# Performance work log

Hardware: AMD Instinct MI355X
Metric: run time of the kernel (lower is better)

Reference implementation:

```python
import jax, jax.numpy as jnp
import numpy as np

D = 1024  # input_size
H = 1024  # hidden_size
B = 128
R = 512


def _lin(x, W, b):
    return x @ W + b


def setup_inputs() -> dict:
    key = jax.random.key(0)
    ks = jax.random.split(key, 20)
    s = 0.02
    inp = {
        "V": jax.random.normal(ks[0], (B, R, D), jnp.float32),
        "s_t": jax.random.normal(ks[1], (B, D), jnp.float32),
        "h_t": jax.random.normal(ks[2], (B, D), jnp.float32),
        # weights stored [in, out] (y = x @ W + b)
        "Wv": jax.random.normal(ks[3], (D, H), jnp.float32) * s,
        "bv": jnp.zeros((H,), jnp.float32),
        "Wsp": jax.random.normal(ks[4], (D, D), jnp.float32) * s,
        "bsp": jnp.zeros((D,), jnp.float32),
        "Wsa": jax.random.normal(ks[5], (D, H), jnp.float32) * s,
        "bsa": jnp.zeros((H,), jnp.float32),
        "Whp": jax.random.normal(ks[6], (D, D), jnp.float32) * s,
        "bhp": jnp.zeros((D,), jnp.float32),
        "Wha": jax.random.normal(ks[7], (D, H), jnp.float32) * s,
        "bha": jnp.zeros((H,), jnp.float32),
        "Wal": jax.random.normal(ks[8], (H, 1), jnp.float32) * s,
        "bal": jnp.zeros((1,), jnp.float32),
        "Wcp": jax.random.normal(ks[9], (D, D), jnp.float32) * s,
        "bcp": jnp.zeros((D,), jnp.float32),
    }
    return inp


def reference(V, s_t, h_t, Wv, bv, Wsp, bsp, Wsa, bsa, Whp, bhp, Wha, bha, Wal, bal, Wcp, bcp):
    v_embed = jax.nn.relu(_lin(V, Wv, bv))           # [B,R,H]
    s_proj = jax.nn.relu(_lin(s_t, Wsp, bsp))        # [B,D]
    s_att = _lin(s_proj, Wsa, bsa)                   # [B,H]
    h_proj = jnp.tanh(_lin(h_t, Whp, bhp))           # [B,D]
    h_att = _lin(h_proj, Wha, bha)                   # [B,H]
    regions = jnp.concatenate([V, s_proj[:, None, :]], axis=1)           # [B,R+1,D]
    regions_att = jnp.concatenate([v_embed, s_att[:, None, :]], axis=1)  # [B,R+1,H]
    alpha_input = jnp.tanh(regions_att + h_att[:, None, :])              # [B,R+1,H]
    scores = (_lin(alpha_input, Wal, bal)).squeeze(-1)                   # [B,R+1]
    alpha = jax.nn.softmax(scores, axis=1)                               # [B,R+1]
    context = jnp.einsum("br,brd->bd", alpha, regions)                   # [B,D]
    z_t = jnp.tanh(_lin(context + h_proj, Wcp, bcp))                     # [B,D]
    return z_t
```

## Files before the change

### kernel.cpp

```cpp
#include <hip/hip_runtime.h>


typedef __bf16 bf16x8 __attribute__((ext_vector_type(8)));
typedef float floatx4 __attribute__((ext_vector_type(4)));

__device__ __forceinline__ float tanh_fast(float x) {
    x = fminf(10.0f, fmaxf(-10.0f, x));
    float e = exp2f(x * 2.885390081777927f);
    return (e - 1.0f) * __builtin_amdgcn_rcpf(e + 1.0f);
}

__global__ __launch_bounds__(256) void conv_k(
    const float* __restrict__ V, __bf16* __restrict__ Vb) {
    const size_t i = ((size_t)blockIdx.x * 256 + threadIdx.x) * 8;
    const float4 a = *reinterpret_cast<const float4*>(V + i);
    const float4 b = *reinterpret_cast<const float4*>(V + i + 4);
    bf16x8 o;
    o[0] = (__bf16)a.x; o[1] = (__bf16)a.y;
    o[2] = (__bf16)a.z; o[3] = (__bf16)a.w;
    o[4] = (__bf16)b.x; o[5] = (__bf16)b.y;
    o[6] = (__bf16)b.z; o[7] = (__bf16)b.w;
    *reinterpret_cast<bf16x8*>(Vb + i) = o;
}

__global__ __launch_bounds__(256) void wvt_kernel(
    const float* __restrict__ Wv, __bf16* __restrict__ WvT) {
    __shared__ float tile[64][65];
    const int k0 = blockIdx.x * 64, n0 = blockIdx.y * 64;
    const int c = threadIdx.x & 63, r = threadIdx.x >> 6;
#pragma unroll
    for (int i = 0; i < 16; ++i)
        tile[r + i * 4][c] = Wv[(size_t)(k0 + r + i * 4) * 1024 + n0 + c];
    __syncthreads();
#pragma unroll
    for (int i = 0; i < 16; ++i)
        WvT[(size_t)(n0 + r + i * 4) * 1024 + k0 + c] =
            (__bf16)tile[c][r + i * 4];
}

__global__ __launch_bounds__(512) void small_gemm_k(
    const float* __restrict__ A0, const float* __restrict__ W0,
    const float* __restrict__ b0, float* __restrict__ C0, int act0,
    const float* __restrict__ A1, const float* __restrict__ W1,
    const float* __restrict__ b1, float* __restrict__ C1, int act1) {
    const float* A; const float* W; const float* bs; float* C; int act;
    if (blockIdx.z == 0) { A = A0; W = W0; bs = b0; C = C0; act = act0; }
    else                 { A = A1; W = W1; bs = b1; C = C1; act = act1; }
    __shared__ float red[3][8][128];
    const int tid = threadIdx.x;
    const int nl = tid & 127, kq = tid >> 7;
    const int n = blockIdx.x * 128 + nl;
    const int m0 = blockIdx.y * 8;
    const float* Ab = A + m0 * 1024;
    float acc[8] = {};
    const int kbeg = kq * 256, kend = kbeg + 256;
#pragma unroll 4
    for (int k = kbeg; k < kend; ++k) {
        float w = W[(size_t)k * 1024 + n];
#pragma unroll
        for (int mi = 0; mi < 8; ++mi)
            acc[mi] = fmaf(Ab[mi * 1024 + k], w, acc[mi]);
    }
    if (kq > 0) {
#pragma unroll
        for (int mi = 0; mi < 8; ++mi) red[kq - 1][mi][nl] = acc[mi];
    }
    __syncthreads();
    if (kq == 0) {
        float bias = bs[n];
#pragma unroll
        for (int mi = 0; mi < 8; ++mi) {
            float v = acc[mi] + red[0][mi][nl] + red[1][mi][nl] +
                      red[2][mi][nl] + bias;
            if (act == 1) v = fmaxf(v, 0.0f);
            else if (act == 2) v = tanh_fast(v);
            C[(size_t)(m0 + mi) * 1024 + n] = v;
        }
    }
}

__global__ __launch_bounds__(256, 3) void score_gemm_k(
    const __bf16* __restrict__ Vb, const __bf16* __restrict__ WvT,
    const float* __restrict__ bv, const float* __restrict__ h_att,
    const float* __restrict__ Wal, float* __restrict__ scores) {
    __shared__ __bf16 As[2][128 * 32];
    __shared__ __bf16 Bs[2][128 * 32];

    const int tid = threadIdx.x;
    const int bid = blockIdx.x;
    const int xcd = bid & 7;
    const int j = bid >> 3;
    const int mtile = xcd * 64 + (j >> 3);
    const int ntile = j & 7;
    const int m0 = mtile * 128, n0 = ntile * 128;
    const int wid = tid >> 6, lane = tid & 63;
    const int wm = wid & 1, wn = wid >> 1;
    const int lcol = lane & 15, quad = lane >> 4;

    floatx4 acc[4][4] = {};

    const int grow = tid >> 2;
    const int kg = (tid & 3) ^ ((grow >> 1) & 3);
    const __bf16* ap0 = Vb + (size_t)(m0 + grow) * 1024 + kg * 8;
    const __bf16* bp0 = WvT + (size_t)(n0 + grow) * 1024 + kg * 8;

    auto dma = [&](int buf, int k0) {
        __builtin_amdgcn_global_load_lds(
            (const __attribute__((address_space(1))) void*)(ap0 + k0),
            (__attribute__((address_space(3))) void*)(&As[buf][tid * 8]),
            16, 0, 0);
        __builtin_amdgcn_global_load_lds(
            (const __attribute__((address_space(1))) void*)(ap0 + 64 * 1024 + k0),
            (__attribute__((address_space(3))) void*)(&As[buf][(256 + tid) * 8]),
            16, 0, 0);
        __builtin_amdgcn_global_load_lds(
            (const __attribute__((address_space(1))) void*)(bp0 + k0),
            (__attribute__((address_space(3))) void*)(&Bs[buf][tid * 8]),
            16, 0, 0);
        __builtin_amdgcn_global_load_lds(
            (const __attribute__((address_space(1))) void*)(bp0 + 64 * 1024 + k0),
            (__attribute__((address_space(3))) void*)(&Bs[buf][(256 + tid) * 8]),
            16, 0, 0);
    };

    dma(0, 0);

    int aoff[4], boff[4];
#pragma unroll
    for (int i = 0; i < 4; ++i) {
        int r = wm * 64 + i * 16 + lcol;
        aoff[i] = r * 32 + ((quad ^ ((r >> 1) & 3)) * 8);
        int n = wn * 64 + i * 16 + lcol;
        boff[i] = n * 32 + ((quad ^ ((n >> 1) & 3)) * 8);
    }
    __syncthreads();

    for (int kk = 0; kk < 32; ++kk) {
        const int cur = kk & 1, nxt = cur ^ 1;
        if (kk < 31) dma(nxt, (kk + 1) * 32);
        bf16x8 af[4], bfr[4];
#pragma unroll
        for (int i = 0; i < 4; ++i) {
            af[i] = *reinterpret_cast<const bf16x8*>(&As[cur][aoff[i]]);
            bfr[i] = *reinterpret_cast<const bf16x8*>(&Bs[cur][boff[i]]);
        }
#pragma unroll
        for (int mi = 0; mi < 4; ++mi)
#pragma unroll
            for (int ni = 0; ni < 4; ++ni)
                acc[mi][ni] = __builtin_amdgcn_mfma_f32_16x16x32_bf16(
                    af[mi], bfr[ni], acc[mi][ni], 0, 0, 0);
        __syncthreads();
    }

    const int b = m0 >> 9;
    float wal[4], hat[4], bvv[4];
#pragma unroll
    for (int ni = 0; ni < 4; ++ni) {
        int n = n0 + wn * 64 + ni * 16 + lcol;
        wal[ni] = Wal[n];
        hat[ni] = h_att[b * 1024 + n];
        bvv[ni] = bv[n];
    }
    float p[16];
#pragma unroll
    for (int mi = 0; mi < 4; ++mi) {
#pragma unroll
        for (int rg = 0; rg < 4; ++rg) {
            float s = 0.f;
#pragma unroll
            for (int ni = 0; ni < 4; ++ni) {
                float x = acc[mi][ni][rg] + bvv[ni];
                x = fmaxf(x, 0.f);
                s = fmaf(wal[ni], tanh_fast(x + hat[ni]), s);
            }
            p[mi * 4 + rg] = s;
        }
    }
#pragma unroll
    for (int off = 1; off < 16; off <<= 1) {
#pragma unroll
        for (int i = 0; i < 16; ++i) p[i] += __shfl_xor(p[i], off, 64);
    }
    if (lcol == 0) {
#pragma unroll
        for (int mi = 0; mi < 4; ++mi)
#pragma unroll
            for (int rg = 0; rg < 4; ++rg) {
                int row = m0 + wm * 64 + mi * 16 + quad * 4 + rg;
                atomicAdd(&scores[b * 513 + (row & 511)], p[mi * 4 + rg]);
            }
    }
}

__global__ __launch_bounds__(256, 3) void score_gemm_fb(
    const float* __restrict__ V, const __bf16* __restrict__ WvT,
    const float* __restrict__ bv, const float* __restrict__ h_att,
    const float* __restrict__ Wal, float* __restrict__ scores) {
    __shared__ __bf16 As[2][128 * 40];
    __shared__ __bf16 Bs[2][128 * 32];

    const int tid = threadIdx.x;
    const int bid = blockIdx.x;
    const int xcd = bid & 7;
    const int j = bid >> 3;
    const int mtile = xcd * 64 + (j >> 3);
    const int ntile = j & 7;
    const int m0 = mtile * 128, n0 = ntile * 128;
    const int wid = tid >> 6, lane = tid & 63;
    const int wm = wid & 1, wn = wid >> 1;
    const int lcol = lane & 15, quad = lane >> 4;

    floatx4 acc[4][4] = {};

    const int am = tid >> 1;
    const int ak = (tid & 1) * 16;
    const float* aptr = V + (size_t)(m0 + am) * 1024 + ak;

    const int g0n = tid >> 2, g0ks = tid & 3;
    const int g1n = (256 + tid) >> 2, g1ks = tid & 3;
    const int g0kg = g0ks ^ ((g0n >> 1) & 3);
    const int g1kg = g1ks ^ ((g1n >> 1) & 3);
    const __bf16* bp0 = WvT + (size_t)(n0 + g0n) * 1024 + g0kg * 8;
    const __bf16* bp1 = WvT + (size_t)(n0 + g1n) * 1024 + g1kg * 8;

    auto stage_A = [&](int buf, float4 f0, float4 f1, float4 f2, float4 f3) {
        bf16x8 u0, u1;
        u0[0] = (__bf16)f0.x; u0[1] = (__bf16)f0.y;
        u0[2] = (__bf16)f0.z; u0[3] = (__bf16)f0.w;
        u0[4] = (__bf16)f1.x; u0[5] = (__bf16)f1.y;
        u0[6] = (__bf16)f1.z; u0[7] = (__bf16)f1.w;
        u1[0] = (__bf16)f2.x; u1[1] = (__bf16)f2.y;
        u1[2] = (__bf16)f2.z; u1[3] = (__bf16)f2.w;
        u1[4] = (__bf16)f3.x; u1[5] = (__bf16)f3.y;
        u1[6] = (__bf16)f3.z; u1[7] = (__bf16)f3.w;
        __bf16* awr = &As[buf][am * 40 + ak];
        *reinterpret_cast<bf16x8*>(awr) = u0;
        *reinterpret_cast<bf16x8*>(awr + 8) = u1;
    };
    auto dma_B = [&](int buf, int k0) {
        __builtin_amdgcn_global_load_lds(
            (const __attribute__((address_space(1))) void*)(bp0 + k0),
            (__attribute__((address_space(3))) void*)(&Bs[buf][tid * 8]),
            16, 0, 0);
        __builtin_amdgcn_global_load_lds(
            (const __attribute__((address_space(1))) void*)(bp1 + k0),
            (__attribute__((address_space(3))) void*)(&Bs[buf][(256 + tid) * 8]),
            16, 0, 0);
    };

    dma_B(0, 0);
    {
        const float4* fp = reinterpret_cast<const float4*>(aptr);
        stage_A(0, fp[0], fp[1], fp[2], fp[3]);
    }
    __syncthreads();

    for (int kk = 0; kk < 32; ++kk) {
        const int cur = kk & 1, nxt = cur ^ 1;
        float4 f0, f1, f2, f3;
        const bool pf = (kk < 31);
        if (pf) {
            dma_B(nxt, (kk + 1) * 32);
            const float4* fp =
                reinterpret_cast<const float4*>(aptr + (kk + 1) * 32);
            f0 = fp[0]; f1 = fp[1]; f2 = fp[2]; f3 = fp[3];
        }
        bf16x8 af[4], bfr[4];
#pragma unroll
        for (int mi = 0; mi < 4; ++mi)
            af[mi] = *reinterpret_cast<const bf16x8*>(
                &As[cur][(wm * 64 + mi * 16 + lcol) * 40 + quad * 8]);
#pragma unroll
        for (int ni = 0; ni < 4; ++ni) {
            int n = wn * 64 + ni * 16 + lcol;
            int ks = quad ^ ((n >> 1) & 3);
            bfr[ni] = *reinterpret_cast<const bf16x8*>(
                &Bs[cur][n * 32 + ks * 8]);
        }
#pragma unroll
        for (int mi = 0; mi < 4; ++mi)
#pragma unroll
            for (int ni = 0; ni < 4; ++ni)
                acc[mi][ni] = __builtin_amdgcn_mfma_f32_16x16x32_bf16(
                    af[mi], bfr[ni], acc[mi][ni], 0, 0, 0);
        if (pf) stage_A(nxt, f0, f1, f2, f3);
        __syncthreads();
    }

    const int b = m0 >> 9;
    float wal[4], hat[4], bvv[4];
#pragma unroll
    for (int ni = 0; ni < 4; ++ni) {
        int n = n0 + wn * 64 + ni * 16 + lcol;
        wal[ni] = Wal[n];
        hat[ni] = h_att[b * 1024 + n];
        bvv[ni] = bv[n];
    }
    float p[16];
#pragma unroll
    for (int mi = 0; mi < 4; ++mi) {
#pragma unroll
        for (int rg = 0; rg < 4; ++rg) {
            float s = 0.f;
#pragma unroll
            for (int ni = 0; ni < 4; ++ni) {
                float x = acc[mi][ni][rg] + bvv[ni];
                x = fmaxf(x, 0.f);
                s = fmaf(wal[ni], tanh_fast(x + hat[ni]), s);
            }
            p[mi * 4 + rg] = s;
        }
    }
#pragma unroll
    for (int off = 1; off < 16; off <<= 1) {
#pragma unroll
        for (int i = 0; i < 16; ++i) p[i] += __shfl_xor(p[i], off, 64);
    }
    if (lcol == 0) {
#pragma unroll
        for (int mi = 0; mi < 4; ++mi)
#pragma unroll
            for (int rg = 0; rg < 4; ++rg) {
                int row = m0 + wm * 64 + mi * 16 + quad * 4 + rg;
                atomicAdd(&scores[b * 513 + (row & 511)], p[mi * 4 + rg]);
            }
    }
}

__global__ __launch_bounds__(256) void lastrow_k(
    const float* __restrict__ s_att, const float* __restrict__ h_att,
    const float* __restrict__ Wal, float* __restrict__ scores) {
    int b = blockIdx.x, tid = threadIdx.x;
    float s = 0.f;
    for (int h = tid; h < 1024; h += 256)
        s += Wal[h] * tanh_fast(s_att[b * 1024 + h] + h_att[b * 1024 + h]);
#pragma unroll
    for (int off = 32; off >= 1; off >>= 1) s += __shfl_xor(s, off, 64);
    __shared__ float red[4];
    if ((tid & 63) == 0) red[tid >> 6] = s;
    __syncthreads();
    if (tid == 0) scores[b * 513 + 512] = red[0] + red[1] + red[2] + red[3];
}

__global__ __launch_bounds__(256) void softmax_k(
    const float* __restrict__ scores, float* __restrict__ alpha) {
    int b = blockIdx.x, tid = threadIdx.x;
    const float* s = scores + b * 513;
    float v0 = s[tid];
    float v1 = s[tid + 256];
    float v2 = (tid == 0) ? s[512] : -1e30f;
    float m = fmaxf(v0, fmaxf(v1, v2));
#pragma unroll
    for (int off = 32; off >= 1; off >>= 1) m = fmaxf(m, __shfl_xor(m, off, 64));
    __shared__ float red[4];
    int w = tid >> 6;
    if ((tid & 63) == 0) red[w] = m;
    __syncthreads();
    m = fmaxf(fmaxf(red[0], red[1]), fmaxf(red[2], red[3]));
    const float L2E = 1.4426950408889634f;
    float e0 = exp2f((v0 - m) * L2E);
    float e1 = exp2f((v1 - m) * L2E);
    float e2 = (tid == 0) ? exp2f((v2 - m) * L2E) : 0.f;
    float sum = e0 + e1 + e2;
#pragma unroll
    for (int off = 32; off >= 1; off >>= 1) sum += __shfl_xor(sum, off, 64);
    __syncthreads();
    if ((tid & 63) == 0) red[w] = sum;
    __syncthreads();
    sum = red[0] + red[1] + red[2] + red[3];
    float inv = 1.0f / sum;
    float* a = alpha + b * 513;
    a[tid] = e0 * inv;
    a[tid + 256] = e1 * inv;
    if (tid == 0) a[512] = e2 * inv;
}

__global__ __launch_bounds__(256) void ctx_k(
    const float* __restrict__ V, const float* __restrict__ alpha,
    const float* __restrict__ s_proj, const float* __restrict__ h_proj,
    float* __restrict__ ctxsum) {
    const int b = blockIdx.x, dq = blockIdx.y;
    const int tid = threadIdx.x;
    const int dl = tid & 63, rq = tid >> 6;
    __shared__ float sal[513];
    __shared__ float red[3][64][4];
    for (int i = tid; i < 513; i += 256) sal[i] = alpha[b * 513 + i];
    __syncthreads();
    const int d0 = dq * 256 + dl * 4;
    const float* vp = V + ((size_t)b * 512 + rq * 128) * 1024 + d0;
    float a0 = 0, a1 = 0, a2 = 0, a3 = 0;
#pragma unroll 8
    for (int r = 0; r < 128; ++r) {
        float al = sal[rq * 128 + r];
        const float4 vv = *reinterpret_cast<const float4*>(vp + (size_t)r * 1024);
        a0 = fmaf(al, vv.x, a0); a1 = fmaf(al, vv.y, a1);
        a2 = fmaf(al, vv.z, a2); a3 = fmaf(al, vv.w, a3);
    }
    if (rq > 0) {
        red[rq - 1][dl][0] = a0; red[rq - 1][dl][1] = a1;
        red[rq - 1][dl][2] = a2; red[rq - 1][dl][3] = a3;
    }
    __syncthreads();
    if (rq == 0) {
#pragma unroll
        for (int q = 0; q < 3; ++q) {
            a0 += red[q][dl][0]; a1 += red[q][dl][1];
            a2 += red[q][dl][2]; a3 += red[q][dl][3];
        }
        float4 sp = *reinterpret_cast<const float4*>(s_proj + b * 1024 + d0);
        float4 hp = *reinterpret_cast<const float4*>(h_proj + b * 1024 + d0);
        float aR = sal[512];
        float4 o;
        o.x = fmaf(aR, sp.x, a0) + hp.x;
        o.y = fmaf(aR, sp.y, a1) + hp.y;
        o.z = fmaf(aR, sp.z, a2) + hp.z;
        o.w = fmaf(aR, sp.w, a3) + hp.w;
        *reinterpret_cast<float4*>(ctxsum + b * 1024 + d0) = o;
    }
}

extern "C" void kernel_launch(void* const* d_in, const int* in_sizes, int n_in,
                              void* d_out, int out_size, void* d_ws,
                              size_t ws_size, hipStream_t stream) {
    const float* V   = (const float*)d_in[0];
    const float* s_t = (const float*)d_in[1];
    const float* h_t = (const float*)d_in[2];
    const float* Wv  = (const float*)d_in[3];
    const float* bv  = (const float*)d_in[4];
    const float* Wsp = (const float*)d_in[5];
    const float* bsp = (const float*)d_in[6];
    const float* Wsa = (const float*)d_in[7];
    const float* bsa = (const float*)d_in[8];
    const float* Whp = (const float*)d_in[9];
    const float* bhp = (const float*)d_in[10];
    const float* Wha = (const float*)d_in[11];
    const float* bha = (const float*)d_in[12];
    const float* Wal = (const float*)d_in[13];
    const float* Wcp = (const float*)d_in[15];
    const float* bcp = (const float*)d_in[16];
    float* out = (float*)d_out;

    const size_t VB_BYTES = (size_t)128 * 512 * 1024 * 2;
    const size_t SMALL_BYTES = 5242880 + 64;
    const bool big = ws_size >= VB_BYTES + SMALL_BYTES;

    char* ws = (char*)d_ws;
    __bf16* Vb = (__bf16*)ws;
    char* base = big ? (ws + VB_BYTES) : ws;
    __bf16* WvT   = (__bf16*)(base + 0);
    float* s_proj = (float*)(base + 2097152);
    float* h_proj = (float*)(base + 2621440);
    float* s_att  = (float*)(base + 3145728);
    float* h_att  = (float*)(base + 3670016);
    float* scores = (float*)(base + 4194304);
    float* alpha  = (float*)(base + 4456960);
    float* ctxsum = (float*)(base + 4719616);

    if (big)
        hipLaunchKernelGGL(conv_k, dim3(32768), dim3(256), 0, stream, V, Vb);
    hipLaunchKernelGGL(wvt_kernel, dim3(16, 16), dim3(256), 0, stream, Wv, WvT);
    hipLaunchKernelGGL(small_gemm_k, dim3(8, 16, 2), dim3(512), 0, stream,
                       s_t, Wsp, bsp, s_proj, 1,
                       h_t, Whp, bhp, h_proj, 2);
    hipLaunchKernelGGL(small_gemm_k, dim3(8, 16, 2), dim3(512), 0, stream,
                       s_proj, Wsa, bsa, s_att, 0,
                       h_proj, Wha, bha, h_att, 0);
    (void)hipMemsetAsync(scores, 0, 128 * 513 * sizeof(float), stream);
    if (big)
        hipLaunchKernelGGL(score_gemm_k, dim3(4096), dim3(256), 0, stream,
                           Vb, WvT, bv, h_att, Wal, scores);
    else
        hipLaunchKernelGGL(score_gemm_fb, dim3(4096), dim3(256), 0, stream,
                           V, WvT, bv, h_att, Wal, scores);
    hipLaunchKernelGGL(lastrow_k, dim3(128), dim3(256), 0, stream,
                       s_att, h_att, Wal, scores);
    hipLaunchKernelGGL(softmax_k, dim3(128), dim3(256), 0, stream,
                       scores, alpha);
    hipLaunchKernelGGL(ctx_k, dim3(128, 4), dim3(256), 0, stream,
                       V, alpha, s_proj, h_proj, ctxsum);
    hipLaunchKernelGGL(small_gemm_k, dim3(8, 16, 1), dim3(512), 0, stream,
                       ctxsum, Wcp, bcp, out, 2,
                       ctxsum, Wcp, bcp, out, 2);
}
```

Measured before the change: 838.8 us.

## Triple-buffer score GEMM loads and read bf16 V copy in context reduction

After: 809.7 us. -3.5%, faster.

```diff
diff --git a/kernel.cpp b/kernel.cpp
--- a/kernel.cpp
+++ b/kernel.cpp
@@ -83,8 +83,8 @@
     const __bf16* __restrict__ Vb, const __bf16* __restrict__ WvT,
     const float* __restrict__ bv, const float* __restrict__ h_att,
     const float* __restrict__ Wal, float* __restrict__ scores) {
-    __shared__ __bf16 As[2][128 * 32];
-    __shared__ __bf16 Bs[2][128 * 32];
+    __shared__ __bf16 As[3][128 * 32];
+    __shared__ __bf16 Bs[3][128 * 32];
 
     const int tid = threadIdx.x;
     const int bid = blockIdx.x;
@@ -124,6 +124,7 @@
     };
 
     dma(0, 0);
+    dma(1, 32);
 
     int aoff[4], boff[4];
 #pragma unroll
@@ -133,11 +134,13 @@
         int n = wn * 64 + i * 16 + lcol;
         boff[i] = n * 32 + ((quad ^ ((n >> 1) & 3)) * 8);
     }
-    __syncthreads();
-
+    asm volatile("s_waitcnt vmcnt(4)" ::: "memory");
+    __builtin_amdgcn_s_barrier();
+
+#pragma unroll
     for (int kk = 0; kk < 32; ++kk) {
-        const int cur = kk & 1, nxt = cur ^ 1;
-        if (kk < 31) dma(nxt, (kk + 1) * 32);
+        const int cur = kk % 3;
+        if (kk < 30) dma((kk + 2) % 3, (kk + 2) * 32);
         bf16x8 af[4], bfr[4];
 #pragma unroll
         for (int i = 0; i < 4; ++i) {
@@ -150,7 +153,13 @@
             for (int ni = 0; ni < 4; ++ni)
                 acc[mi][ni] = __builtin_amdgcn_mfma_f32_16x16x32_bf16(
                     af[mi], bfr[ni], acc[mi][ni], 0, 0, 0);
-        __syncthreads();
+        if (kk < 30) {
+            asm volatile("s_waitcnt vmcnt(4)" ::: "memory");
+            __builtin_amdgcn_s_barrier();
+        } else if (kk == 30) {
+            asm volatile("s_waitcnt vmcnt(0)" ::: "memory");
+            __builtin_amdgcn_s_barrier();
+        }
     }
 
     const int b = m0 >> 9;
@@ -377,6 +386,56 @@
 }
 
 __global__ __launch_bounds__(256) void ctx_k(
+    const __bf16* __restrict__ Vb, const float* __restrict__ alpha,
+    const float* __restrict__ s_proj, const float* __restrict__ h_proj,
+    float* __restrict__ ctxsum) {
+    const int b = blockIdx.x, dq = blockIdx.y;
+    const int tid = threadIdx.x;
+    const int dl = tid & 63, rq = tid >> 6;
+    __shared__ float sal[513];
+    __shared__ float red[3][64][9];
+    for (int i = tid; i < 513; i += 256) sal[i] = alpha[b * 513 + i];
+    __syncthreads();
+    const int d0 = dq * 512 + dl * 8;
+    const __bf16* vp = Vb + ((size_t)b * 512 + rq * 128) * 1024 + d0;
+    float a[8] = {};
+#pragma unroll 4
+    for (int r = 0; r < 128; ++r) {
+        float al = sal[rq * 128 + r];
+        bf16x8 vv = *reinterpret_cast<const bf16x8*>(vp + (size_t)r * 1024);
+#pragma unroll
+        for (int jj = 0; jj < 8; ++jj) a[jj] = fmaf(al, (float)vv[jj], a[jj]);
+    }
+    if (rq > 0) {
+#pragma unroll
+        for (int jj = 0; jj < 8; ++jj) red[rq - 1][dl][jj] = a[jj];
+    }
+    __syncthreads();
+    if (rq == 0) {
+#pragma unroll
+        for (int q = 0; q < 3; ++q)
+#pragma unroll
+            for (int jj = 0; jj < 8; ++jj) a[jj] += red[q][dl][jj];
+        float aR = sal[512];
+        float4 sp0 = *reinterpret_cast<const float4*>(s_proj + b * 1024 + d0);
+        float4 sp1 = *reinterpret_cast<const float4*>(s_proj + b * 1024 + d0 + 4);
+        float4 hp0 = *reinterpret_cast<const float4*>(h_proj + b * 1024 + d0);
+        float4 hp1 = *reinterpret_cast<const float4*>(h_proj + b * 1024 + d0 + 4);
+        float4 o0, o1;
+        o0.x = fmaf(aR, sp0.x, a[0]) + hp0.x;
+        o0.y = fmaf(aR, sp0.y, a[1]) + hp0.y;
+        o0.z = fmaf(aR, sp0.z, a[2]) + hp0.z;
+        o0.w = fmaf(aR, sp0.w, a[3]) + hp0.w;
+        o1.x = fmaf(aR, sp1.x, a[4]) + hp1.x;
+        o1.y = fmaf(aR, sp1.y, a[5]) + hp1.y;
+        o1.z = fmaf(aR, sp1.z, a[6]) + hp1.z;
+        o1.w = fmaf(aR, sp1.w, a[7]) + hp1.w;
+        *reinterpret_cast<float4*>(ctxsum + b * 1024 + d0) = o0;
+        *reinterpret_cast<float4*>(ctxsum + b * 1024 + d0 + 4) = o1;
+    }
+}
+
+__global__ __launch_bounds__(256) void ctx_fb(
     const float* __restrict__ V, const float* __restrict__ alpha,
     const float* __restrict__ s_proj, const float* __restrict__ h_proj,
     float* __restrict__ ctxsum) {
@@ -477,8 +536,12 @@
                        s_att, h_att, Wal, scores);
     hipLaunchKernelGGL(softmax_k, dim3(128), dim3(256), 0, stream,
                        scores, alpha);
-    hipLaunchKernelGGL(ctx_k, dim3(128, 4), dim3(256), 0, stream,
-                       V, alpha, s_proj, h_proj, ctxsum);
+    if (big)
+        hipLaunchKernelGGL(ctx_k, dim3(128, 2), dim3(256), 0, stream,
+                           Vb, alpha, s_proj, h_proj, ctxsum);
+    else
+        hipLaunchKernelGGL(ctx_fb, dim3(128, 4), dim3(256), 0, stream,
+                           V, alpha, s_proj, h_proj, ctxsum);
     hipLaunchKernelGGL(small_gemm_k, dim3(8, 16, 1), dim3(512), 0, stream,
                        ctxsum, Wcp, bcp, out, 2,
                        ctxsum, Wcp, bcp, out, 2);
```
